# Kernel tuning notes

Measured on AMD Instinct MI355X. Metric: run time of the kernel, lower is better.

Reference implementation:

```python
import jax, jax.numpy as jnp
import numpy as np

HIDDEN = 1024
HEADS = 16
HEAD_DIM = HIDDEN // HEADS


def setup_inputs() -> dict:
    key = jax.random.key(0)
    ks = jax.random.split(key, 9)
    B, S = 2, 2048
    std = 0.02
    inp = {
        "query": jax.random.normal(ks[0], (B, S, HIDDEN), dtype=jnp.float32),
        "Wq": jax.random.normal(ks[1], (HIDDEN, HIDDEN), dtype=jnp.float32) * std,
        "bq": jnp.zeros((HIDDEN,), dtype=jnp.float32),
        "Wk": jax.random.normal(ks[2], (HIDDEN, HIDDEN), dtype=jnp.float32) * std,
        "bk": jnp.zeros((HIDDEN,), dtype=jnp.float32),
        "Wv": jax.random.normal(ks[3], (HIDDEN, HIDDEN), dtype=jnp.float32) * std,
        "bv": jnp.zeros((HIDDEN,), dtype=jnp.float32),
        "Wo": jax.random.normal(ks[4], (HIDDEN, HIDDEN), dtype=jnp.float32) * std,
        "bo": jnp.zeros((HIDDEN,), dtype=jnp.float32),
    }
    return inp


def reference(query, Wq, bq, Wk, bk, Wv, bv, Wo, bo):
    B, S, H = query.shape
    # torch nn.Linear: y = x @ W.T + b
    Q = query @ Wq.T + bq
    K = query @ Wk.T + bk  # key defaults to query (self-attention)
    V = query @ Wv.T + bv
    # [B, S, H] -> [B, heads, S, head_dim]
    def split_heads(x):
        return x.reshape(B, S, HEADS, HEAD_DIM).transpose(0, 2, 1, 3)
    Qh, Kh, Vh = split_heads(Q), split_heads(K), split_heads(V)
    scale = jnp.sqrt(jnp.asarray(HEAD_DIM, dtype=query.dtype))
    scores = jnp.einsum("bhqd,bhkd->bhqk", Qh, Kh) / scale
    attn = jax.nn.softmax(scores, axis=-1)  # dropout=0 (eval)
    context = jnp.einsum("bhqk,bhkd->bhqd", attn, Vh)
    context = context.transpose(0, 2, 1, 3).reshape(B, S, H)
    output = context @ Wo.T + bo
    return output, attn
```

## Files before the change

### kernel.cpp

```cpp
#include <hip/hip_runtime.h>
#include <hip/hip_bf16.h>
#include <cstdint>

typedef __attribute__((ext_vector_type(4))) float f32x4;
typedef __attribute__((ext_vector_type(8))) short bf16x8;

__device__ __forceinline__ unsigned short f2bf(float f){
  union { float f; unsigned int u; } v; v.f = f;
  unsigned int u = v.u;
  u += 0x7FFFu + ((u >> 16) & 1u);
  return (unsigned short)(u >> 16);
}

__global__ __launch_bounds__(256) void cvt_bf16(const float* __restrict__ in,
                                                unsigned short* __restrict__ out,
                                                int n4){
  int i = blockIdx.x * 256 + threadIdx.x;
  if (i < n4){
    float4 v = ((const float4*)in)[i];
    ushort4 o;
    o.x = f2bf(v.x); o.y = f2bf(v.y); o.z = f2bf(v.z); o.w = f2bf(v.w);
    ((ushort4*)out)[i] = o;
  }
}

__global__ __launch_bounds__(256) void gemm_bt(
    const unsigned short* __restrict__ A,
    const unsigned short* __restrict__ Bw,
    const float* __restrict__ bias,
    void* __restrict__ outp,
    int M, int N, int K, int mode)
{
  __shared__ unsigned short As[2][128*64];
  __shared__ unsigned short Bs[2][128*64];

  const int tid = threadIdx.x;
  const int l   = tid & 63;
  const int wid = tid >> 6;
  const int g   = l >> 4;
  const int li  = l & 15;
  const int m0  = blockIdx.y * 128;
  const int n0  = blockIdx.x * 128;
  const int wm  = (wid >> 1) * 64;
  const int wn  = (wid & 1) * 64;
  const int srow = tid >> 3;
  const int sck  = tid & 7;

  const unsigned short* Ag = A  + (size_t)(m0 + srow) * K + sck * 8;
  const unsigned short* Bg = Bw + (size_t)(n0 + srow) * K + sck * 8;

  f32x4 acc[4][4] = {};
  bf16x8 ra[4], rb[4];
  const int NT = K >> 6;

  #pragma unroll
  for (int r = 0; r < 4; ++r){
    ra[r] = *(const bf16x8*)(Ag + (size_t)(r*32) * K);
    rb[r] = *(const bf16x8*)(Bg + (size_t)(r*32) * K);
  }
  #pragma unroll
  for (int r = 0; r < 4; ++r){
    const int row = srow + r*32;
    const int ck  = sck ^ (row & 7);
    *(bf16x8*)(&As[0][row*64 + ck*8]) = ra[r];
    *(bf16x8*)(&Bs[0][row*64 + ck*8]) = rb[r];
  }
  __syncthreads();

  int cur = 0;
  for (int kt = 0; kt < NT; ++kt){
    if (kt + 1 < NT){
      const int kof = (kt + 1) << 6;
      #pragma unroll
      for (int r = 0; r < 4; ++r){
        ra[r] = *(const bf16x8*)(Ag + (size_t)(r*32) * K + kof);
        rb[r] = *(const bf16x8*)(Bg + (size_t)(r*32) * K + kof);
      }
    }
    #pragma unroll
    for (int kk = 0; kk < 2; ++kk){
      bf16x8 af[4], bfr[4];
      #pragma unroll
      for (int f = 0; f < 4; ++f){
        const int rowa = wm + f*16 + li;
        const int cka  = (kk*4 + g) ^ (rowa & 7);
        af[f] = *(const bf16x8*)(&As[cur][rowa*64 + cka*8]);
        const int rowb = wn + f*16 + li;
        const int ckb  = (kk*4 + g) ^ (rowb & 7);
        bfr[f] = *(const bf16x8*)(&Bs[cur][rowb*64 + ckb*8]);
      }
      #pragma unroll
      for (int fm = 0; fm < 4; ++fm)
        #pragma unroll
        for (int fn = 0; fn < 4; ++fn)
          acc[fm][fn] = __builtin_amdgcn_mfma_f32_16x16x32_bf16(af[fm], bfr[fn], acc[fm][fn], 0, 0, 0);
    }
    __syncthreads();
    if (kt + 1 < NT){
      #pragma unroll
      for (int r = 0; r < 4; ++r){
        const int row = srow + r*32;
        const int ck  = sck ^ (row & 7);
        *(bf16x8*)(&As[cur^1][row*64 + ck*8]) = ra[r];
        *(bf16x8*)(&Bs[cur^1][row*64 + ck*8]) = rb[r];
      }
      __syncthreads();
    }
    cur ^= 1;
  }

  #pragma unroll
  for (int fn = 0; fn < 4; ++fn){
    const int col = n0 + wn + fn*16 + li;
    const float bv = bias[col];
    #pragma unroll
    for (int fm = 0; fm < 4; ++fm){
      #pragma unroll
      for (int j = 0; j < 4; ++j){
        const int row = m0 + wm + fm*16 + g*4 + j;
        const float v = acc[fm][fn][j] + bv;
        if (mode == 0){
          ((unsigned short*)outp)[(size_t)row * N + col] = f2bf(v);
        } else if (mode == 1){
          const int bb = row >> 11;
          const int s  = row & 2047;
          ((unsigned short*)outp)[((size_t)(bb*1024 + col)) * 2048 + s] = f2bf(v);
        } else {
          ((float*)outp)[(size_t)row * N + col] = v;
        }
      }
    }
  }
}

__global__ __launch_bounds__(512, 4) void attn_fused(
    const unsigned short* __restrict__ Qb,
    const unsigned short* __restrict__ Kb,
    const unsigned short* __restrict__ Vt,
    float* __restrict__ attn,
    unsigned short* __restrict__ ctxb)
{
  __shared__ float red[128];
  __shared__ __align__(16) unsigned short Pb[16 * 2048];
  float* ctxred = (float*)Pb;
  char*  Pbb    = (char*)Pb;

  const int tid = threadIdx.x;
  const int l   = tid & 63;
  const int w   = tid >> 6;
  const int g   = l >> 4;
  const int li  = l & 15;
  const int q0  = blockIdx.x * 16;
  const int bh  = blockIdx.y;
  const int b   = bh >> 4;
  const int h   = bh & 15;

  const size_t qrow = (size_t)(b*2048 + q0 + li) * 1024 + h*64 + g*8;
  const bf16x8 aq0 = *(const bf16x8*)(Qb + qrow);
  const bf16x8 aq1 = *(const bf16x8*)(Qb + qrow + 32);

  const unsigned short* Kbase = Kb + (size_t)(b*2048) * 1024 + h*64 + g*8;

  f32x4 s[16];
  #pragma unroll
  for (int cf = 0; cf < 16; ++cf){
    const unsigned short* kr = Kbase + (size_t)(w*256 + cf*16 + li) * 1024;
    const bf16x8 bk0 = *(const bf16x8*)(kr);
    const bf16x8 bk1 = *(const bf16x8*)(kr + 32);
    f32x4 t = {};
    t = __builtin_amdgcn_mfma_f32_16x16x32_bf16(bk0, aq0, t, 0, 0, 0);
    t = __builtin_amdgcn_mfma_f32_16x16x32_bf16(bk1, aq1, t, 0, 0, 0);
    s[cf] = t;
  }

  float ls = 0.f;
  const int swz = li << 3;
  #pragma unroll
  for (int cf = 0; cf < 16; ++cf){
    f32x4 t = s[cf];
    #pragma unroll
    for (int j = 0; j < 4; ++j){
      const float p = __expf(t[j] * 0.125f);
      t[j] = p;
      ls += p;
    }
    s[cf] = t;
    ushort4 u;
    u.x = f2bf(t[0]); u.y = f2bf(t[1]); u.z = f2bf(t[2]); u.w = f2bf(t[3]);
    const int colb = w*512 + cf*32 + g*8;
    *(ushort4*)(Pbb + li*4096 + (colb ^ swz)) = u;
  }

  ls += __shfl_xor(ls, 16);
  ls += __shfl_xor(ls, 32);
  if (l < 16) red[w*16 + l] = ls;
  __syncthreads();

  float dli = 0.f;
  #pragma unroll
  for (int ww = 0; ww < 8; ++ww) dli += red[ww*16 + li];
  const float rinv = 1.0f / dli;
  float r4[4];
  #pragma unroll
  for (int j = 0; j < 4; ++j){
    float dj = 0.f;
    #pragma unroll
    for (int ww = 0; ww < 8; ++ww) dj += red[ww*16 + g*4 + j];
    r4[j] = 1.0f / dj;
  }

  {
    float* abase = attn + ((size_t)bh * 2048 + q0 + li) * 2048 + w*256;
    #pragma unroll
    for (int cf = 0; cf < 16; ++cf){
      f32x4 o;
      o[0] = s[cf][0]*rinv; o[1] = s[cf][1]*rinv;
      o[2] = s[cf][2]*rinv; o[3] = s[cf][3]*rinv;
      __builtin_nontemporal_store(o, (f32x4*)(abase + cf*16 + g*4));
    }
  }

  f32x4 pv[4] = {};
  const unsigned short* Vbase = Vt + (size_t)(b*1024 + h*64) * 2048 + w*256;
  #pragma unroll
  for (int kt = 0; kt < 8; ++kt){
    const int colb2 = w*512 + kt*64 + g*16;
    const ushort4 plo = *(const ushort4*)(Pbb + li*4096 + ( colb2      ^ swz));
    const ushort4 phi = *(const ushort4*)(Pbb + li*4096 + ((colb2 + 8) ^ swz));
    bf16x8 pa;
    pa[0] = plo.x; pa[1] = plo.y; pa[2] = plo.z; pa[3] = plo.w;
    pa[4] = phi.x; pa[5] = phi.y; pa[6] = phi.z; pa[7] = phi.w;
    #pragma unroll
    for (int df = 0; df < 4; ++df){
      const bf16x8 vb = *(const bf16x8*)(Vbase + (size_t)(df*16 + li) * 2048 + kt*32 + g*8);
      pv[df] = __builtin_amdgcn_mfma_f32_16x16x32_bf16(pa, vb, pv[df], 0, 0, 0);
    }
  }

  __syncthreads();
  #pragma unroll
  for (int df = 0; df < 4; ++df){
    #pragma unroll
    for (int j = 0; j < 4; ++j)
      ctxred[w*1024 + (g*4 + j)*64 + df*16 + li] = pv[df][j] * r4[j];
  }
  __syncthreads();
  {
    const int idx = tid * 2;
    const int r = idx >> 6;
    const int d = idx & 63;
    float v0 = 0.f, v1 = 0.f;
    #pragma unroll
    for (int ww = 0; ww < 8; ++ww){
      v0 += ctxred[ww*1024 + r*64 + d];
      v1 += ctxred[ww*1024 + r*64 + d + 1];
    }
    const unsigned int packed = (unsigned int)f2bf(v0) | ((unsigned int)f2bf(v1) << 16);
    *(unsigned int*)(ctxb + (size_t)(b*2048 + q0 + r) * 1024 + h*64 + d) = packed;
  }
}

extern "C" void kernel_launch(void* const* d_in, const int* in_sizes, int n_in,
                              void* d_out, int out_size, void* d_ws, size_t ws_size,
                              hipStream_t stream)
{
  const float* X  = (const float*)d_in[0];
  const float* Wq = (const float*)d_in[1];
  const float* bq = (const float*)d_in[2];
  const float* Wk = (const float*)d_in[3];
  const float* bk = (const float*)d_in[4];
  const float* Wv = (const float*)d_in[5];
  const float* bv = (const float*)d_in[6];
  const float* Wo = (const float*)d_in[7];
  const float* bo = (const float*)d_in[8];

  char* ws = (char*)d_ws;
  unsigned short* Xb  = (unsigned short*)(ws);
  unsigned short* Qb  = (unsigned short*)(ws + (size_t)( 8u<<20));
  unsigned short* Kbf = (unsigned short*)(ws + (size_t)(16u<<20));
  unsigned short* Vt  = (unsigned short*)(ws + (size_t)(24u<<20));
  unsigned short* Cb  = (unsigned short*)(ws + (size_t)(32u<<20));
  unsigned short* Wqb = (unsigned short*)(ws + (size_t)(40u<<20));
  unsigned short* Wkb = (unsigned short*)(ws + (size_t)(42u<<20));
  unsigned short* Wvb = (unsigned short*)(ws + (size_t)(44u<<20));
  unsigned short* Wob = (unsigned short*)(ws + (size_t)(46u<<20));

  float* out  = (float*)d_out;
  float* attn = out + (size_t)4194304;

  cvt_bf16<<<4096, 256, 0, stream>>>(X,  Xb,  1048576);
  cvt_bf16<<<1024, 256, 0, stream>>>(Wq, Wqb, 262144);
  cvt_bf16<<<1024, 256, 0, stream>>>(Wk, Wkb, 262144);
  cvt_bf16<<<1024, 256, 0, stream>>>(Wv, Wvb, 262144);
  cvt_bf16<<<1024, 256, 0, stream>>>(Wo, Wob, 262144);

  dim3 ggrid(8, 32);
  gemm_bt<<<ggrid, 256, 0, stream>>>(Xb, Wqb, bq, Qb,  4096, 1024, 1024, 0);
  gemm_bt<<<ggrid, 256, 0, stream>>>(Xb, Wkb, bk, Kbf, 4096, 1024, 1024, 0);
  gemm_bt<<<ggrid, 256, 0, stream>>>(Xb, Wvb, bv, Vt,  4096, 1024, 1024, 1);

  dim3 agrid(128, 32);
  attn_fused<<<agrid, 512, 0, stream>>>(Qb, Kbf, Vt, attn, Cb);

  gemm_bt<<<ggrid, 256, 0, stream>>>(Cb, Wob, bo, out, 4096, 1024, 1024, 2);
}
```

Baseline: 386.4 us.

## Fuse QKV projections into one launch and re-read attn probs from LDS

The three Q/K/V projection GEMMs become a single kernel launch with a 24x32 grid that picks the weight, bias and output layout per block. This removes two launches and fills the GPU better with 768 blocks. In the attention kernel, the fp32 probabilities are no longer held in registers across the PV MFMA loop. They are re-read from the bf16 P tile in LDS and written row-contiguous after the PV product, which lowers register pressure and makes the attn stores coalesced. The trade-off is that the stored attn values are now bf16-rounded before normalisation, which reduces their precision.

```diff
diff --git a/kernel.cpp b/kernel.cpp
--- a/kernel.cpp
+++ b/kernel.cpp
@@ -10,6 +10,10 @@
   unsigned int u = v.u;
   u += 0x7FFFu + ((u >> 16) & 1u);
   return (unsigned short)(u >> 16);
+}
+__device__ __forceinline__ float bf2f(unsigned short s){
+  union { unsigned int u; float f; } v; v.u = ((unsigned int)s) << 16;
+  return v.f;
 }
 
 __global__ __launch_bounds__(256) void cvt_bf16(const float* __restrict__ in,
@@ -24,12 +28,130 @@
   }
 }
 
+__global__ __launch_bounds__(256) void qkv_gemm(
+    const unsigned short* __restrict__ A,
+    const unsigned short* __restrict__ W0,
+    const unsigned short* __restrict__ W1,
+    const unsigned short* __restrict__ W2,
+    const float* __restrict__ b0,
+    const float* __restrict__ b1,
+    const float* __restrict__ b2,
+    unsigned short* __restrict__ Qo,
+    unsigned short* __restrict__ Ko,
+    unsigned short* __restrict__ Vto)
+{
+  __shared__ unsigned short As[2][128*64];
+  __shared__ unsigned short Bs[2][128*64];
+
+  const int K = 1024;
+  const int tid = threadIdx.x;
+  const int l   = tid & 63;
+  const int wid = tid >> 6;
+  const int g   = l >> 4;
+  const int li  = l & 15;
+  const int widx = blockIdx.x >> 3;
+  const int m0  = blockIdx.y * 128;
+  const int n0  = (blockIdx.x & 7) * 128;
+  const int wm  = (wid >> 1) * 64;
+  const int wn  = (wid & 1) * 64;
+  const int srow = tid >> 3;
+  const int sck  = tid & 7;
+
+  const unsigned short* Bw = (widx == 0) ? W0 : ((widx == 1) ? W1 : W2);
+  const float* bias        = (widx == 0) ? b0 : ((widx == 1) ? b1 : b2);
+
+  const unsigned short* Ag = A  + (size_t)(m0 + srow) * K + sck * 8;
+  const unsigned short* Bg = Bw + (size_t)(n0 + srow) * K + sck * 8;
+
+  f32x4 acc[4][4] = {};
+  bf16x8 ra[4], rb[4];
+  const int NT = K >> 6;
+
+  #pragma unroll
+  for (int r = 0; r < 4; ++r){
+    ra[r] = *(const bf16x8*)(Ag + (size_t)(r*32) * K);
+    rb[r] = *(const bf16x8*)(Bg + (size_t)(r*32) * K);
+  }
+  #pragma unroll
+  for (int r = 0; r < 4; ++r){
+    const int row = srow + r*32;
+    const int ck  = sck ^ (row & 7);
+    *(bf16x8*)(&As[0][row*64 + ck*8]) = ra[r];
+    *(bf16x8*)(&Bs[0][row*64 + ck*8]) = rb[r];
+  }
+  __syncthreads();
+
+  int cur = 0;
+  for (int kt = 0; kt < NT; ++kt){
+    if (kt + 1 < NT){
+      const int kof = (kt + 1) << 6;
+      #pragma unroll
+      for (int r = 0; r < 4; ++r){
+        ra[r] = *(const bf16x8*)(Ag + (size_t)(r*32) * K + kof);
+        rb[r] = *(const bf16x8*)(Bg + (size_t)(r*32) * K + kof);
+      }
+    }
+    #pragma unroll
+    for (int kk = 0; kk < 2; ++kk){
+      bf16x8 af[4], bfr[4];
+      #pragma unroll
+      for (int f = 0; f < 4; ++f){
+        const int rowa = wm + f*16 + li;
+        const int cka  = (kk*4 + g) ^ (rowa & 7);
+        af[f] = *(const bf16x8*)(&As[cur][rowa*64 + cka*8]);
+        const int rowb = wn + f*16 + li;
+        const int ckb  = (kk*4 + g) ^ (rowb & 7);
+        bfr[f] = *(const bf16x8*)(&Bs[cur][rowb*64 + ckb*8]);
+      }
+      #pragma unroll
+      for (int fm = 0; fm < 4; ++fm)
+        #pragma unroll
+        for (int fn = 0; fn < 4; ++fn)
+          acc[fm][fn] = __builtin_amdgcn_mfma_f32_16x16x32_bf16(af[fm], bfr[fn], acc[fm][fn], 0, 0, 0);
+    }
+    __syncthreads();
+    if (kt + 1 < NT){
+      #pragma unroll
+      for (int r = 0; r < 4; ++r){
+        const int row = srow + r*32;
+        const int ck  = sck ^ (row & 7);
+        *(bf16x8*)(&As[cur^1][row*64 + ck*8]) = ra[r];
+        *(bf16x8*)(&Bs[cur^1][row*64 + ck*8]) = rb[r];
+      }
+      __syncthreads();
+    }
+    cur ^= 1;
+  }
+
+  unsigned short* Oqk = (widx == 0) ? Qo : Ko;
+  #pragma unroll
+  for (int fn = 0; fn < 4; ++fn){
+    const int col = n0 + wn + fn*16 + li;
+    const float bv = bias[col];
+    #pragma unroll
+    for (int fm = 0; fm < 4; ++fm){
+      #pragma unroll
+      for (int j = 0; j < 4; ++j){
+        const int row = m0 + wm + fm*16 + g*4 + j;
+        const float v = acc[fm][fn][j] + bv;
+        if (widx < 2){
+          Oqk[(size_t)row * 1024 + col] = f2bf(v);
+        } else {
+          const int bb = row >> 11;
+          const int s  = row & 2047;
+          Vto[((size_t)(bb*1024 + col)) * 2048 + s] = f2bf(v);
+        }
+      }
+    }
+  }
+}
+
 __global__ __launch_bounds__(256) void gemm_bt(
     const unsigned short* __restrict__ A,
     const unsigned short* __restrict__ Bw,
     const float* __restrict__ bias,
-    void* __restrict__ outp,
-    int M, int N, int K, int mode)
+    float* __restrict__ outp,
+    int M, int N, int K)
 {
   __shared__ unsigned short As[2][128*64];
   __shared__ unsigned short Bs[2][128*64];
@@ -118,16 +240,7 @@
       #pragma unroll
       for (int j = 0; j < 4; ++j){
         const int row = m0 + wm + fm*16 + g*4 + j;
-        const float v = acc[fm][fn][j] + bv;
-        if (mode == 0){
-          ((unsigned short*)outp)[(size_t)row * N + col] = f2bf(v);
-        } else if (mode == 1){
-          const int bb = row >> 11;
-          const int s  = row & 2047;
-          ((unsigned short*)outp)[((size_t)(bb*1024 + col)) * 2048 + s] = f2bf(v);
-        } else {
-          ((float*)outp)[(size_t)row * N + col] = v;
-        }
+        outp[(size_t)row * N + col] = acc[fm][fn][j] + bv;
       }
     }
   }
@@ -177,16 +290,13 @@
   const int swz = li << 3;
   #pragma unroll
   for (int cf = 0; cf < 16; ++cf){
-    f32x4 t = s[cf];
-    #pragma unroll
-    for (int j = 0; j < 4; ++j){
-      const float p = __expf(t[j] * 0.125f);
-      t[j] = p;
-      ls += p;
-    }
-    s[cf] = t;
+    float p0 = __expf(s[cf][0] * 0.125f);
+    float p1 = __expf(s[cf][1] * 0.125f);
+    float p2 = __expf(s[cf][2] * 0.125f);
+    float p3 = __expf(s[cf][3] * 0.125f);
+    ls += p0 + p1 + p2 + p3;
     ushort4 u;
-    u.x = f2bf(t[0]); u.y = f2bf(t[1]); u.z = f2bf(t[2]); u.w = f2bf(t[3]);
+    u.x = f2bf(p0); u.y = f2bf(p1); u.z = f2bf(p2); u.w = f2bf(p3);
     const int colb = w*512 + cf*32 + g*8;
     *(ushort4*)(Pbb + li*4096 + (colb ^ swz)) = u;
   }
@@ -196,10 +306,6 @@
   if (l < 16) red[w*16 + l] = ls;
   __syncthreads();
 
-  float dli = 0.f;
-  #pragma unroll
-  for (int ww = 0; ww < 8; ++ww) dli += red[ww*16 + li];
-  const float rinv = 1.0f / dli;
   float r4[4];
   #pragma unroll
   for (int j = 0; j < 4; ++j){
@@ -207,17 +313,6 @@
     #pragma unroll
     for (int ww = 0; ww < 8; ++ww) dj += red[ww*16 + g*4 + j];
     r4[j] = 1.0f / dj;
-  }
-
-  {
-    float* abase = attn + ((size_t)bh * 2048 + q0 + li) * 2048 + w*256;
-    #pragma unroll
-    for (int cf = 0; cf < 16; ++cf){
-      f32x4 o;
-      o[0] = s[cf][0]*rinv; o[1] = s[cf][1]*rinv;
-      o[2] = s[cf][2]*rinv; o[3] = s[cf][3]*rinv;
-      __builtin_nontemporal_store(o, (f32x4*)(abase + cf*16 + g*4));
-    }
   }
 
   f32x4 pv[4] = {};
@@ -234,6 +329,28 @@
     for (int df = 0; df < 4; ++df){
       const bf16x8 vb = *(const bf16x8*)(Vbase + (size_t)(df*16 + li) * 2048 + kt*32 + g*8);
       pv[df] = __builtin_amdgcn_mfma_f32_16x16x32_bf16(pa, vb, pv[df], 0, 0, 0);
+    }
+  }
+
+  {
+    #pragma unroll
+    for (int rr = 0; rr < 2; ++rr){
+      const int r = 2*w + rr;
+      float dj = 0.f;
+      #pragma unroll
+      for (int ww = 0; ww < 8; ++ww) dj += red[ww*16 + r];
+      const float rv = 1.0f / dj;
+      const int key = r << 3;
+      float* arow = attn + ((size_t)bh * 2048 + q0 + r) * 2048;
+      #pragma unroll
+      for (int c0 = 0; c0 < 8; ++c0){
+        const int cb = c0*512 + l*8;
+        const ushort4 u = *(const ushort4*)(Pbb + r*4096 + (cb ^ key));
+        f32x4 o;
+        o[0] = bf2f(u.x) * rv; o[1] = bf2f(u.y) * rv;
+        o[2] = bf2f(u.z) * rv; o[3] = bf2f(u.w) * rv;
+        __builtin_nontemporal_store(o, (f32x4*)(arow + c0*256 + l*4));
+      }
     }
   }
 
@@ -294,13 +411,12 @@
   cvt_bf16<<<1024, 256, 0, stream>>>(Wv, Wvb, 262144);
   cvt_bf16<<<1024, 256, 0, stream>>>(Wo, Wob, 262144);
 
-  dim3 ggrid(8, 32);
-  gemm_bt<<<ggrid, 256, 0, stream>>>(Xb, Wqb, bq, Qb,  4096, 1024, 1024, 0);
-  gemm_bt<<<ggrid, 256, 0, stream>>>(Xb, Wkb, bk, Kbf, 4096, 1024, 1024, 0);
-  gemm_bt<<<ggrid, 256, 0, stream>>>(Xb, Wvb, bv, Vt,  4096, 1024, 1024, 1);
+  dim3 qkvgrid(24, 32);
+  qkv_gemm<<<qkvgrid, 256, 0, stream>>>(Xb, Wqb, Wkb, Wvb, bq, bk, bv, Qb, Kbf, Vt);
 
   dim3 agrid(128, 32);
   attn_fused<<<agrid, 512, 0, stream>>>(Qb, Kbf, Vt, attn, Cb);
 
-  gemm_bt<<<ggrid, 256, 0, stream>>>(Cb, Wob, bo, out, 4096, 1024, 1024, 2);
-}
+  dim3 ggrid(8, 32);
+  gemm_bt<<<ggrid, 256, 0, stream>>>(Cb, Wob, bo, out, 4096, 1024, 1024);
+}
```

Result: faster. 346.7 us (-10.3%).
